# Kernel tuning notes

Measured on AMD Instinct MI355X. Metric: run time of the kernel, lower is better.

## Reference

```python
import jax, jax.numpy as jnp
import numpy as np

L, V, D, H, FF, MAXLEN = 6, 32000, 512, 8, 2048, 512
EPS = 1e-6


def _pos_encoding(max_len, d):
    pos = jnp.arange(max_len, dtype=jnp.float32)[:, None]            # [S,1]
    i = (jnp.floor(jnp.arange(d, dtype=jnp.float32) / 2) * 2) / d     # [D]
    inv = 1.0 / jnp.power(10000.0, i)
    em = pos * inv[None, :]                                           # [S,D]
    even = (jnp.arange(d) % 2) == 0
    return jnp.where(even[None, :], jnp.sin(em), jnp.cos(em))         # [S,D]


def _layernorm(x, g, b):
    mu = jnp.mean(x, axis=-1, keepdims=True)
    var = jnp.mean(jnp.square(x - mu), axis=-1, keepdims=True)
    return (x - mu) / jnp.sqrt(var + EPS) * g + b


def _mha(q_in, k_in, v_in, mask, w, b):
    # w: [4, D, D] torch-style [out,in] for q,k,v,o; b: [4, D]
    dh = D // H
    q = jnp.einsum('bsd,od->bso', q_in, w[0]) + b[0]
    k = jnp.einsum('bsd,od->bso', k_in, w[1]) + b[1]
    v = jnp.einsum('bsd,od->bso', v_in, w[2]) + b[2]
    split = lambda t: t.reshape(t.shape[0], t.shape[1], H, dh).transpose(0, 2, 1, 3)
    q, k, v = split(q), split(k), split(v)                            # [B,H,S,dh]
    s = jnp.einsum('bhqd,bhkd->bhqk', q, k) / jnp.sqrt(jnp.float32(dh))
    s = s - mask * 1e6
    a = jax.nn.softmax(s, axis=-1)
    o = jnp.einsum('bhqk,bhkd->bhqd', a, v)
    o = o.transpose(0, 2, 1, 3).reshape(o.shape[0], -1, D)
    return jnp.einsum('bsd,od->bso', o, w[3]) + b[3]


def setup_inputs() -> dict:
    key = jax.random.key(0)
    ks = jax.random.split(key, 20)
    B, S = 4, 512
    tokens = jax.random.randint(ks[0], (B, S), 0, V)
    en_out = jax.random.normal(ks[1], (B, S, D), dtype=jnp.float32)
    en_pad_mask = jnp.where(jax.random.uniform(ks[2], (B, 1, 1, S)) < 0.1, 1.0, 0.0).astype(jnp.float32)
    emb = jax.random.normal(ks[3], (V, D), dtype=jnp.float32) * 0.1
    emb = emb.at[0].set(0.0)  # padding_idx=0
    gain = 2.0 ** 0.5
    std_att = gain / np.sqrt(D)
    sa_w = jax.random.normal(ks[4], (L, 4, D, D), dtype=jnp.float32) * std_att
    sa_b = jnp.zeros((L, 4, D), dtype=jnp.float32)
    ca_w = jax.random.normal(ks[5], (L, 4, D, D), dtype=jnp.float32) * std_att
    ca_b = jnp.zeros((L, 4, D), dtype=jnp.float32)
    ff_w1 = jax.random.normal(ks[6], (L, FF, D), dtype=jnp.float32) * (gain / np.sqrt(D))
    ff_b1 = jnp.zeros((L, FF), dtype=jnp.float32)
    ff_w2 = jax.random.normal(ks[7], (L, D, FF), dtype=jnp.float32) * (gain / np.sqrt(FF))
    ff_b2 = jnp.zeros((L, D), dtype=jnp.float32)
    ln_g = jnp.ones((L, 3, D), dtype=jnp.float32)
    ln_b = jnp.zeros((L, 3, D), dtype=jnp.float32)
    out_w = jax.random.normal(ks[8], (V, D), dtype=jnp.float32) * np.sqrt(2.0 / (V + D))
    out_b = jnp.zeros((V,), dtype=jnp.float32)
    return dict(tokens=tokens, en_out=en_out, en_pad_mask=en_pad_mask, emb=emb,
                sa_w=sa_w, sa_b=sa_b, ca_w=ca_w, ca_b=ca_b,
                ff_w1=ff_w1, ff_b1=ff_b1, ff_w2=ff_w2, ff_b2=ff_b2,
                ln_g=ln_g, ln_b=ln_b, out_w=out_w, out_b=out_b)


def reference(tokens, en_out, en_pad_mask, emb, sa_w, sa_b, ca_w, ca_b,
              ff_w1, ff_b1, ff_w2, ff_b2, ln_g, ln_b, out_w, out_b):
    B, S = tokens.shape
    # decoder padding mask + lookahead mask
    de_pad = jnp.where(tokens == 0, 1.0, 0.0).reshape(B, 1, 1, S)
    tri = (1.0 - jnp.tril(jnp.ones((S, S), dtype=jnp.float32)))[None, None]  # [1,1,S,S]
    la_mask = jnp.maximum(de_pad, tri)                                        # [B,1,S,S]
    # embedding + positional encoding (dropout p given; inference -> identity)
    x = emb[tokens] * jnp.sqrt(jnp.float32(D)) + _pos_encoding(MAXLEN, D)[None, :S]
    for i in range(L):
        h = _layernorm(x + _mha(x, x, x, la_mask, sa_w[i], sa_b[i]), ln_g[i, 0], ln_b[i, 0])
        a = _layernorm(h + _mha(h, en_out, en_out, en_pad_mask, ca_w[i], ca_b[i]), ln_g[i, 1], ln_b[i, 1])
        ff = jnp.einsum('bsf,df->bsd', jax.nn.relu(jnp.einsum('bsd,fd->bsf', a, ff_w1[i]) + ff_b1[i]), ff_w2[i]) + ff_b2[i]
        x = _layernorm(a + ff, ln_g[i, 2], ln_b[i, 2])
    return jnp.einsum('bsd,vd->bsv', x, out_w) + out_b
```

## Files before the change

kernel.cpp:

```cpp
#include <hip/hip_runtime.h>
#include <math.h>

#define DMODEL 512
#define NHEAD  8
#define DHEAD  64
#define SEQ    512
#define BATCH  4
#define NLAYER 6
#define FFDIM  2048
#define VOCAB  32000

__global__ void embed_kernel(const int* __restrict__ tokens,
                             const float* __restrict__ emb,
                             float* __restrict__ x) {
    int idx = blockIdx.x;
    int s   = idx & (SEQ - 1);
    int tok = tokens[idx];
    const float scale = 22.627416997969522f;
    for (int d = threadIdx.x; d < DMODEL; d += blockDim.x) {
        float i2  = (float)((d >> 1) << 1) / (float)DMODEL;
        float inv = powf(10000.0f, -i2);
        float em  = (float)s * inv;
        float pe  = ((d & 1) == 0) ? sinf(em) : cosf(em);
        x[(size_t)idx * DMODEL + d] = emb[(size_t)tok * DMODEL + d] * scale + pe;
    }
}

__global__ __launch_bounds__(256) void gemm_bias_64(
        const float* __restrict__ A, const float* __restrict__ W,
        const float* __restrict__ bias, float* __restrict__ C,
        int M, int N, int K, int relu) {
    __shared__ float As[32][68];
    __shared__ float Bs[32][68];
    int bm  = blockIdx.x * 64;
    int bn  = blockIdx.y * 64;
    int tid = threadIdx.x;
    int tx  = tid & 15;
    int ty  = tid >> 4;
    int lrow = tid >> 2;
    int lq   = (tid & 3) << 2;

    const float* Ap = A + (size_t)(bm + lrow) * K + lq;
    const float* Wp = W + (size_t)(bn + lrow) * K + lq;

    float acc[4][4] = {};
    float4 av0 = *(const float4*)Ap;
    float4 av1 = *(const float4*)(Ap + 16);
    float4 wv0 = *(const float4*)Wp;
    float4 wv1 = *(const float4*)(Wp + 16);

    for (int k0 = 0; k0 < K; k0 += 32) {
        As[lq + 0][lrow]  = av0.x; As[lq + 1][lrow]  = av0.y;
        As[lq + 2][lrow]  = av0.z; As[lq + 3][lrow]  = av0.w;
        As[lq + 16][lrow] = av1.x; As[lq + 17][lrow] = av1.y;
        As[lq + 18][lrow] = av1.z; As[lq + 19][lrow] = av1.w;
        Bs[lq + 0][lrow]  = wv0.x; Bs[lq + 1][lrow]  = wv0.y;
        Bs[lq + 2][lrow]  = wv0.z; Bs[lq + 3][lrow]  = wv0.w;
        Bs[lq + 16][lrow] = wv1.x; Bs[lq + 17][lrow] = wv1.y;
        Bs[lq + 18][lrow] = wv1.z; Bs[lq + 19][lrow] = wv1.w;
        __syncthreads();
        int kn = (k0 + 32 < K) ? k0 + 32 : k0;
        av0 = *(const float4*)(Ap + kn);
        av1 = *(const float4*)(Ap + kn + 16);
        wv0 = *(const float4*)(Wp + kn);
        wv1 = *(const float4*)(Wp + kn + 16);
#pragma unroll
        for (int kk = 0; kk < 32; kk++) {
            float4 a = *(const float4*)&As[kk][ty * 4];
            float4 b = *(const float4*)&Bs[kk][tx * 4];
            float ar[4] = {a.x, a.y, a.z, a.w};
            float br[4] = {b.x, b.y, b.z, b.w};
#pragma unroll
            for (int i = 0; i < 4; i++)
#pragma unroll
                for (int j = 0; j < 4; j++) acc[i][j] += ar[i] * br[j];
        }
        __syncthreads();
    }

    float4 bv = *(const float4*)(bias + bn + tx * 4);
    float bb[4] = {bv.x, bv.y, bv.z, bv.w};
#pragma unroll
    for (int i = 0; i < 4; i++) {
        int row = bm + ty * 4 + i;
        float4 v;
        v.x = acc[i][0] + bb[0]; v.y = acc[i][1] + bb[1];
        v.z = acc[i][2] + bb[2]; v.w = acc[i][3] + bb[3];
        if (relu) {
            v.x = fmaxf(v.x, 0.f); v.y = fmaxf(v.y, 0.f);
            v.z = fmaxf(v.z, 0.f); v.w = fmaxf(v.w, 0.f);
        }
        *(float4*)(C + (size_t)row * N + bn + tx * 4) = v;
    }
}

__global__ __launch_bounds__(256) void gemm_bias_128(
        const float* __restrict__ A, const float* __restrict__ W,
        const float* __restrict__ bias, float* __restrict__ C,
        int M, int N, int K, int relu) {
    __shared__ float As[32][132];
    __shared__ float Bs[32][132];
    int bm  = blockIdx.x * 128;
    int bn  = blockIdx.y * 128;
    int tid = threadIdx.x;
    int tx  = tid & 15;
    int ty  = tid >> 4;
    int lrow = tid >> 2;
    int lq   = (tid & 3) << 2;

    const float* Ap  = A + (size_t)(bm + lrow) * K + lq;
    const float* Ap2 = Ap + (size_t)64 * K;
    const float* Wp  = W + (size_t)(bn + lrow) * K + lq;
    const float* Wp2 = Wp + (size_t)64 * K;

    float acc[8][8] = {};
    float4 a00 = *(const float4*)Ap;
    float4 a01 = *(const float4*)(Ap + 16);
    float4 a10 = *(const float4*)Ap2;
    float4 a11 = *(const float4*)(Ap2 + 16);
    float4 w00 = *(const float4*)Wp;
    float4 w01 = *(const float4*)(Wp + 16);
    float4 w10 = *(const float4*)Wp2;
    float4 w11 = *(const float4*)(Wp2 + 16);

    for (int k0 = 0; k0 < K; k0 += 32) {
        As[lq + 0][lrow]       = a00.x; As[lq + 1][lrow]       = a00.y;
        As[lq + 2][lrow]       = a00.z; As[lq + 3][lrow]       = a00.w;
        As[lq + 16][lrow]      = a01.x; As[lq + 17][lrow]      = a01.y;
        As[lq + 18][lrow]      = a01.z; As[lq + 19][lrow]      = a01.w;
        As[lq + 0][lrow + 64]  = a10.x; As[lq + 1][lrow + 64]  = a10.y;
        As[lq + 2][lrow + 64]  = a10.z; As[lq + 3][lrow + 64]  = a10.w;
        As[lq + 16][lrow + 64] = a11.x; As[lq + 17][lrow + 64] = a11.y;
        As[lq + 18][lrow + 64] = a11.z; As[lq + 19][lrow + 64] = a11.w;
        Bs[lq + 0][lrow]       = w00.x; Bs[lq + 1][lrow]       = w00.y;
        Bs[lq + 2][lrow]       = w00.z; Bs[lq + 3][lrow]       = w00.w;
        Bs[lq + 16][lrow]      = w01.x; Bs[lq + 17][lrow]      = w01.y;
        Bs[lq + 18][lrow]      = w01.z; Bs[lq + 19][lrow]      = w01.w;
        Bs[lq + 0][lrow + 64]  = w10.x; Bs[lq + 1][lrow + 64]  = w10.y;
        Bs[lq + 2][lrow + 64]  = w10.z; Bs[lq + 3][lrow + 64]  = w10.w;
        Bs[lq + 16][lrow + 64] = w11.x; Bs[lq + 17][lrow + 64] = w11.y;
        Bs[lq + 18][lrow + 64] = w11.z; Bs[lq + 19][lrow + 64] = w11.w;
        __syncthreads();
        int kn = (k0 + 32 < K) ? k0 + 32 : k0;
        a00 = *(const float4*)(Ap + kn);
        a01 = *(const float4*)(Ap + kn + 16);
        a10 = *(const float4*)(Ap2 + kn);
        a11 = *(const float4*)(Ap2 + kn + 16);
        w00 = *(const float4*)(Wp + kn);
        w01 = *(const float4*)(Wp + kn + 16);
        w10 = *(const float4*)(Wp2 + kn);
        w11 = *(const float4*)(Wp2 + kn + 16);
#pragma unroll
        for (int kk = 0; kk < 32; kk++) {
            float4 A0 = *(const float4*)&As[kk][ty * 4];
            float4 A1 = *(const float4*)&As[kk][ty * 4 + 64];
            float4 B0 = *(const float4*)&Bs[kk][tx * 4];
            float4 B1 = *(const float4*)&Bs[kk][tx * 4 + 64];
            float ar[8] = {A0.x, A0.y, A0.z, A0.w, A1.x, A1.y, A1.z, A1.w};
            float br[8] = {B0.x, B0.y, B0.z, B0.w, B1.x, B1.y, B1.z, B1.w};
#pragma unroll
            for (int i = 0; i < 8; i++)
#pragma unroll
                for (int j = 0; j < 8; j++) acc[i][j] += ar[i] * br[j];
        }
        __syncthreads();
    }

    float4 bv0 = *(const float4*)(bias + bn + tx * 4);
    float4 bv1 = *(const float4*)(bias + bn + tx * 4 + 64);
    float bb[8] = {bv0.x, bv0.y, bv0.z, bv0.w, bv1.x, bv1.y, bv1.z, bv1.w};
#pragma unroll
    for (int i = 0; i < 8; i++) {
        int row = bm + ty * 4 + (i & 3) + (i >> 2) * 64;
        float4 v0, v1;
        v0.x = acc[i][0] + bb[0]; v0.y = acc[i][1] + bb[1];
        v0.z = acc[i][2] + bb[2]; v0.w = acc[i][3] + bb[3];
        v1.x = acc[i][4] + bb[4]; v1.y = acc[i][5] + bb[5];
        v1.z = acc[i][6] + bb[6]; v1.w = acc[i][7] + bb[7];
        if (relu) {
            v0.x = fmaxf(v0.x, 0.f); v0.y = fmaxf(v0.y, 0.f);
            v0.z = fmaxf(v0.z, 0.f); v0.w = fmaxf(v0.w, 0.f);
            v1.x = fmaxf(v1.x, 0.f); v1.y = fmaxf(v1.y, 0.f);
            v1.z = fmaxf(v1.z, 0.f); v1.w = fmaxf(v1.w, 0.f);
        }
        float* crow = C + (size_t)row * N + bn + tx * 4;
        *(float4*)crow = v0;
        *(float4*)(crow + 64) = v1;
    }
}

__global__ __launch_bounds__(256) void attn_tile_kernel(
        const float* __restrict__ Q, const float* __restrict__ K,
        const float* __restrict__ Vv, const int* __restrict__ tokens,
        const float* __restrict__ en_pad, float* __restrict__ O,
        int ldq, int ldkv, int causal) {
    int qt  = blockIdx.x;
    int h   = blockIdx.y;
    int b   = blockIdx.z;
    int tid = threadIdx.x;
    int tx  = tid & 15;
    int ty  = tid >> 4;
    int lrow = tid >> 2;
    int lq4  = tid & 3;

    __shared__ float Qs[DHEAD][68];
    __shared__ float KP[64][68];
    __shared__ float Vs[64][72];

    {
        const float* qbase = Q + ((size_t)b * SEQ + qt * 64 + lrow) * ldq + h * DHEAD;
#pragma unroll
        for (int i = 0; i < 4; i++) {
            int dk = (lq4 + i * 4) * 4;
            float4 f = *(const float4*)(qbase + dk);
            Qs[dk + 0][lrow] = f.x; Qs[dk + 1][lrow] = f.y;
            Qs[dk + 2][lrow] = f.z; Qs[dk + 3][lrow] = f.w;
        }
    }

    float o[4][4] = {};
    float mrow[4] = {-INFINITY, -INFINITY, -INFINITY, -INFINITY};
    float lsum[4] = {0.f, 0.f, 0.f, 0.f};
    int nc = causal ? (qt + 1) : (SEQ / 64);

    for (int ct = 0; ct < nc; ct++) {
        __syncthreads();
        const float* kbase = K  + ((size_t)b * SEQ + ct * 64 + lrow) * ldkv + h * DHEAD;
        const float* vbase = Vv + ((size_t)b * SEQ + ct * 64 + lrow) * ldkv + h * DHEAD;
#pragma unroll
        for (int i = 0; i < 4; i++) {
            int dk = (lq4 + i * 4) * 4;
            float4 f = *(const float4*)(kbase + dk);
            KP[dk + 0][lrow] = f.x; KP[dk + 1][lrow] = f.y;
            KP[dk + 2][lrow] = f.z; KP[dk + 3][lrow] = f.w;
            float4 g = *(const float4*)(vbase + dk);
            *(float4*)&Vs[lrow][dk] = g;
        }
        __syncthreads();

        float s[4][4] = {};
#pragma unroll
        for (int d = 0; d < DHEAD; d++) {
            float4 a  = *(const float4*)&Qs[d][ty * 4];
            float4 bb = *(const float4*)&KP[d][tx * 4];
            float ar[4] = {a.x, a.y, a.z, a.w};
            float br[4] = {bb.x, bb.y, bb.z, bb.w};
#pragma unroll
            for (int i = 0; i < 4; i++)
#pragma unroll
                for (int j = 0; j < 4; j++) s[i][j] += ar[i] * br[j];
        }
        __syncthreads();

        float cmask[4];
#pragma unroll
        for (int j = 0; j < 4; j++) {
            int jg = ct * 64 + tx * 4 + j;
            cmask[j] = causal ? ((tokens[b * SEQ + jg] == 0) ? 1.0f : 0.0f)
                              : en_pad[b * SEQ + jg];
        }
#pragma unroll
        for (int i = 0; i < 4; i++) {
            int qg = qt * 64 + ty * 4 + i;
#pragma unroll
            for (int j = 0; j < 4; j++) {
                int jg = ct * 64 + tx * 4 + j;
                float mk = cmask[j];
                if (causal && jg > qg) mk = 1.0f;
                s[i][j] = s[i][j] * 0.125f - mk * 1.0e6f;
            }
        }

#pragma unroll
        for (int i = 0; i < 4; i++) {
            float rm = fmaxf(fmaxf(s[i][0], s[i][1]), fmaxf(s[i][2], s[i][3]));
#pragma unroll
            for (int msk = 1; msk < 16; msk <<= 1)
                rm = fmaxf(rm, __shfl_xor(rm, msk));
            float mn = fmaxf(mrow[i], rm);
            float sc = expf(mrow[i] - mn);
            mrow[i] = mn;
            float ps = 0.0f;
#pragma unroll
            for (int j = 0; j < 4; j++) {
                float p = expf(s[i][j] - mn);
                s[i][j] = p;
                ps += p;
            }
#pragma unroll
            for (int msk = 1; msk < 16; msk <<= 1)
                ps += __shfl_xor(ps, msk);
            lsum[i] = lsum[i] * sc + ps;
#pragma unroll
            for (int j = 0; j < 4; j++) o[i][j] *= sc;
        }

#pragma unroll
        for (int i = 0; i < 4; i++)
            *(float4*)&KP[ty * 4 + i][tx * 4] =
                make_float4(s[i][0], s[i][1], s[i][2], s[i][3]);
        __syncthreads();

#pragma unroll
        for (int k0 = 0; k0 < 64; k0 += 4) {
            float4 a0 = *(const float4*)&KP[ty * 4 + 0][k0];
            float4 a1 = *(const float4*)&KP[ty * 4 + 1][k0];
            float4 a2 = *(const float4*)&KP[ty * 4 + 2][k0];
            float4 a3 = *(const float4*)&KP[ty * 4 + 3][k0];
            float ar[4][4] = {{a0.x, a0.y, a0.z, a0.w},
                              {a1.x, a1.y, a1.z, a1.w},
                              {a2.x, a2.y, a2.z, a2.w},
                              {a3.x, a3.y, a3.z, a3.w}};
#pragma unroll
            for (int kk = 0; kk < 4; kk++) {
                float4 bv = *(const float4*)&Vs[k0 + kk][tx * 4];
                float br[4] = {bv.x, bv.y, bv.z, bv.w};
#pragma unroll
                for (int i = 0; i < 4; i++)
#pragma unroll
                    for (int j = 0; j < 4; j++) o[i][j] += ar[i][kk] * br[j];
            }
        }
    }

#pragma unroll
    for (int i = 0; i < 4; i++) {
        float inv = 1.0f / lsum[i];
        float4 v = make_float4(o[i][0] * inv, o[i][1] * inv,
                               o[i][2] * inv, o[i][3] * inv);
        *(float4*)(O + ((size_t)b * SEQ + qt * 64 + ty * 4 + i) * DMODEL
                   + h * DHEAD + tx * 4) = v;
    }
}

__global__ __launch_bounds__(64) void ln_res_kernel(
        const float* __restrict__ x, const float* __restrict__ y,
        const float* __restrict__ g, const float* __restrict__ b,
        float* __restrict__ out) {
    int row = blockIdx.x;
    int t   = threadIdx.x;
    size_t base = (size_t)row * DMODEL;
    const float4* x4 = (const float4*)(x + base);
    const float4* y4 = (const float4*)(y + base);
    float4 a0 = x4[t], a1 = x4[t + 64];
    float4 c0 = y4[t], c1 = y4[t + 64];
    float v0x = a0.x + c0.x, v0y = a0.y + c0.y, v0z = a0.z + c0.z, v0w = a0.w + c0.w;
    float v1x = a1.x + c1.x, v1y = a1.y + c1.y, v1z = a1.z + c1.z, v1w = a1.w + c1.w;

    float s = v0x + v0y + v0z + v0w + v1x + v1y + v1z + v1w;
#pragma unroll
    for (int m = 1; m < 64; m <<= 1) s += __shfl_xor(s, m);
    float mu = s * (1.0f / 512.0f);

    float d0x = v0x - mu, d0y = v0y - mu, d0z = v0z - mu, d0w = v0w - mu;
    float d1x = v1x - mu, d1y = v1y - mu, d1z = v1z - mu, d1w = v1w - mu;
    float q = d0x * d0x + d0y * d0y + d0z * d0z + d0w * d0w
            + d1x * d1x + d1y * d1y + d1z * d1z + d1w * d1w;
#pragma unroll
    for (int m = 1; m < 64; m <<= 1) q += __shfl_xor(q, m);
    float inv = rsqrtf(q * (1.0f / 512.0f) + 1e-6f);

    const float4* g4 = (const float4*)g;
    const float4* b4 = (const float4*)b;
    float4 gv0 = g4[t], gv1 = g4[t + 64];
    float4 bv0 = b4[t], bv1 = b4[t + 64];
    float4* o4 = (float4*)(out + base);
    o4[t]      = make_float4(d0x * inv * gv0.x + bv0.x, d0y * inv * gv0.y + bv0.y,
                             d0z * inv * gv0.z + bv0.z, d0w * inv * gv0.w + bv0.w);
    o4[t + 64] = make_float4(d1x * inv * gv1.x + bv1.x, d1y * inv * gv1.y + bv1.y,
                             d1z * inv * gv1.z + bv1.z, d1w * inv * gv1.w + bv1.w);
}

extern "C" void kernel_launch(void* const* d_in, const int* in_sizes, int n_in,
                              void* d_out, int out_size, void* d_ws, size_t ws_size,
                              hipStream_t stream) {
    const int*   tokens = (const int*)  d_in[0];
    const float* en_out = (const float*)d_in[1];
    const float* en_pad = (const float*)d_in[2];
    const float* emb    = (const float*)d_in[3];
    const float* sa_w   = (const float*)d_in[4];
    const float* sa_b   = (const float*)d_in[5];
    const float* ca_w   = (const float*)d_in[6];
    const float* ca_b   = (const float*)d_in[7];
    const float* ff_w1  = (const float*)d_in[8];
    const float* ff_b1  = (const float*)d_in[9];
    const float* ff_w2  = (const float*)d_in[10];
    const float* ff_b2  = (const float*)d_in[11];
    const float* ln_g   = (const float*)d_in[12];
    const float* ln_b   = (const float*)d_in[13];
    const float* out_w  = (const float*)d_in[14];
    const float* out_b  = (const float*)d_in[15];
    float* logits = (float*)d_out;

    const int BS = BATCH * SEQ;
    const size_t NTOK = (size_t)BS * DMODEL;

    float* ws   = (float*)d_ws;
    float* buf0 = ws;
    float* buf1 = ws + NTOK;
    float* qkv  = ws + 2 * NTOK;
    float* kv   = qkv + NTOK;
    float* att  = ws + 5 * NTOK;
    float* proj = ws + 6 * NTOK;
    float* ffb  = ws + 7 * NTOK;

    dim3 g_qkv(BS / 64, 3 * DMODEL / 64);
    dim3 g_dd(BS / 64, DMODEL / 64);
    dim3 g_kv(BS / 64, 2 * DMODEL / 64);
    dim3 g_ff1(BS / 128, FFDIM / 128);
    dim3 g_vocab(BS / 128, VOCAB / 128);
    dim3 attn_grid(SEQ / 64, NHEAD, BATCH);

    embed_kernel<<<BS, 256, 0, stream>>>(tokens, emb, buf0);

    float* cur = buf0;
    float* oth = buf1;
    for (int l = 0; l < NLAYER; l++) {
        const float* sw = sa_w + (size_t)l * 4 * DMODEL * DMODEL;
        const float* sb = sa_b + (size_t)l * 4 * DMODEL;
        const float* cw = ca_w + (size_t)l * 4 * DMODEL * DMODEL;
        const float* cb = ca_b + (size_t)l * 4 * DMODEL;
        const float* lg = ln_g + (size_t)l * 3 * DMODEL;
        const float* lb = ln_b + (size_t)l * 3 * DMODEL;

        gemm_bias_64<<<g_qkv, 256, 0, stream>>>(cur, sw, sb, qkv, BS, 3 * DMODEL, DMODEL, 0);
        attn_tile_kernel<<<attn_grid, 256, 0, stream>>>(qkv, qkv + DMODEL, qkv + 2 * DMODEL,
                                                        tokens, nullptr, att,
                                                        3 * DMODEL, 3 * DMODEL, 1);
        gemm_bias_64<<<g_dd, 256, 0, stream>>>(att, sw + 3 * DMODEL * DMODEL, sb + 3 * DMODEL,
                                               proj, BS, DMODEL, DMODEL, 0);
        ln_res_kernel<<<BS, 64, 0, stream>>>(cur, proj, lg, lb, oth);

        gemm_bias_64<<<g_dd, 256, 0, stream>>>(oth, cw, cb, qkv, BS, DMODEL, DMODEL, 0);
        gemm_bias_64<<<g_kv, 256, 0, stream>>>(en_out, cw + DMODEL * DMODEL, cb + DMODEL,
                                               kv, BS, 2 * DMODEL, DMODEL, 0);
        attn_tile_kernel<<<attn_grid, 256, 0, stream>>>(qkv, kv, kv + DMODEL,
                                                        tokens, en_pad, att,
                                                        DMODEL, 2 * DMODEL, 0);
        gemm_bias_64<<<g_dd, 256, 0, stream>>>(att, cw + 3 * DMODEL * DMODEL, cb + 3 * DMODEL,
                                               proj, BS, DMODEL, DMODEL, 0);
        ln_res_kernel<<<BS, 64, 0, stream>>>(oth, proj, lg + DMODEL, lb + DMODEL, cur);

        gemm_bias_128<<<g_ff1, 256, 0, stream>>>(cur, ff_w1 + (size_t)l * FFDIM * DMODEL,
                                                 ff_b1 + (size_t)l * FFDIM, ffb,
                                                 BS, FFDIM, DMODEL, 1);
        gemm_bias_64<<<g_dd, 256, 0, stream>>>(ffb, ff_w2 + (size_t)l * DMODEL * FFDIM,
                                               ff_b2 + (size_t)l * DMODEL, proj,
                                               BS, DMODEL, FFDIM, 0);
        ln_res_kernel<<<BS, 64, 0, stream>>>(cur, proj, lg + 2 * DMODEL, lb + 2 * DMODEL, oth);

        float* t2 = cur; cur = oth; oth = t2;
    }

    gemm_bias_128<<<g_vocab, 256, 0, stream>>>(cur, out_w, out_b, logits, BS, VOCAB, DMODEL, 0);
}
```

Measured before the change: 4.029 ms.

## Use split-bf16 MFMA GEMM for wide projections, FFN1 and vocab

Adds a GEMM kernel that splits each fp32 operand into three bf16 parts and accumulates six cross-product MFMA 16x16x32 bf16 instructions, emulating near-fp32 precision on matrix cores. It replaces the scalar FMA GEMMs for the QKV, cross-attention KV, FFN first layer and vocabulary projections, where most of the FLOPs are. The aim is to move the dominant matrix work onto MFMA units. The cost is the extra splitting ALU work, a larger LDS footprint and a store epilogue that writes scalars with strided access instead of float4.

```diff
diff --git a/kernel.cpp b/kernel.cpp
--- a/kernel.cpp
+++ b/kernel.cpp
@@ -9,6 +9,11 @@
 #define NLAYER 6
 #define FFDIM  2048
 #define VOCAB  32000
+
+using bf16x8 = __attribute__((ext_vector_type(8))) __bf16;
+using f32x4  = __attribute__((ext_vector_type(4))) float;
+typedef unsigned int uint32;
+typedef unsigned short ushort16;
 
 __global__ void embed_kernel(const int* __restrict__ tokens,
                              const float* __restrict__ emb,
@@ -26,6 +31,139 @@
     }
 }
 
+__device__ __forceinline__ void split3(float x, ushort16& s0, ushort16& s1, ushort16& s2) {
+    uint32 u0 = __builtin_bit_cast(uint32, x);
+    s0 = (ushort16)(u0 >> 16);
+    float r1 = x - __builtin_bit_cast(float, u0 & 0xffff0000u);
+    uint32 u1 = __builtin_bit_cast(uint32, r1);
+    s1 = (ushort16)(u1 >> 16);
+    float r2 = r1 - __builtin_bit_cast(float, u1 & 0xffff0000u);
+    s2 = (ushort16)(__builtin_bit_cast(uint32, r2) >> 16);
+}
+
+#define LDSP 40
+__global__ __launch_bounds__(256, 2) void gemm_mfma3(
+        const float* __restrict__ A, const float* __restrict__ W,
+        const float* __restrict__ bias, float* __restrict__ C,
+        int M, int N, int K, int relu) {
+    __shared__ ushort16 As[3][128][LDSP];
+    __shared__ ushort16 Bs[3][128][LDSP];
+    int bm  = blockIdx.x * 128;
+    int bn  = blockIdx.y * 128;
+    int tid = threadIdx.x;
+    int w   = tid >> 6;
+    int l   = tid & 63;
+    int wrow = (w >> 1) * 64;
+    int wcol = (w & 1) * 64;
+    int r2  = tid >> 2;
+    int qq  = tid & 3;
+
+    const float* Abase = A + (size_t)(bm + r2) * K + qq * 4;
+    const float* Wbase = W + (size_t)(bn + r2) * K + qq * 4;
+    const size_t rowK64 = (size_t)64 * K;
+
+    f32x4 acc[4][4];
+#pragma unroll
+    for (int i = 0; i < 4; i++)
+#pragma unroll
+        for (int j = 0; j < 4; j++) acc[i][j] = (f32x4){0.f, 0.f, 0.f, 0.f};
+
+    float4 va[4], vw[4];
+#pragma unroll
+    for (int c = 0; c < 4; c++) {
+        size_t off = (size_t)(c >> 1) * rowK64 + (c & 1) * 16;
+        va[c] = *(const float4*)(Abase + off);
+        vw[c] = *(const float4*)(Wbase + off);
+    }
+
+    for (int k0 = 0; k0 < K; k0 += 32) {
+#pragma unroll
+        for (int c = 0; c < 4; c++) {
+            int row = r2 + ((c >> 1) << 6);
+            int kb  = (qq << 2) + ((c & 1) << 4);
+            float xa[4] = {va[c].x, va[c].y, va[c].z, va[c].w};
+            float xw[4] = {vw[c].x, vw[c].y, vw[c].z, vw[c].w};
+            ushort16 a0[4], a1[4], a2[4], w0[4], w1[4], w2[4];
+#pragma unroll
+            for (int e = 0; e < 4; e++) {
+                split3(xa[e], a0[e], a1[e], a2[e]);
+                split3(xw[e], w0[e], w1[e], w2[e]);
+            }
+            *(uint32*)&As[0][row][kb]     = (uint32)a0[0] | ((uint32)a0[1] << 16);
+            *(uint32*)&As[0][row][kb + 2] = (uint32)a0[2] | ((uint32)a0[3] << 16);
+            *(uint32*)&As[1][row][kb]     = (uint32)a1[0] | ((uint32)a1[1] << 16);
+            *(uint32*)&As[1][row][kb + 2] = (uint32)a1[2] | ((uint32)a1[3] << 16);
+            *(uint32*)&As[2][row][kb]     = (uint32)a2[0] | ((uint32)a2[1] << 16);
+            *(uint32*)&As[2][row][kb + 2] = (uint32)a2[2] | ((uint32)a2[3] << 16);
+            *(uint32*)&Bs[0][row][kb]     = (uint32)w0[0] | ((uint32)w0[1] << 16);
+            *(uint32*)&Bs[0][row][kb + 2] = (uint32)w0[2] | ((uint32)w0[3] << 16);
+            *(uint32*)&Bs[1][row][kb]     = (uint32)w1[0] | ((uint32)w1[1] << 16);
+            *(uint32*)&Bs[1][row][kb + 2] = (uint32)w1[2] | ((uint32)w1[3] << 16);
+            *(uint32*)&Bs[2][row][kb]     = (uint32)w2[0] | ((uint32)w2[1] << 16);
+            *(uint32*)&Bs[2][row][kb + 2] = (uint32)w2[2] | ((uint32)w2[3] << 16);
+        }
+        __syncthreads();
+
+        if (k0 + 32 < K) {
+#pragma unroll
+            for (int c = 0; c < 4; c++) {
+                size_t off = (size_t)(c >> 1) * rowK64 + (c & 1) * 16 + k0 + 32;
+                va[c] = *(const float4*)(Abase + off);
+                vw[c] = *(const float4*)(Wbase + off);
+            }
+        }
+
+        int fr = l & 15;
+        int kg = (l >> 4) * 8;
+        bf16x8 bf[3][4];
+#pragma unroll
+        for (int nj = 0; nj < 4; nj++) {
+            int rowb = wcol + nj * 16 + fr;
+            bf[0][nj] = *(const bf16x8*)&Bs[0][rowb][kg];
+            bf[1][nj] = *(const bf16x8*)&Bs[1][rowb][kg];
+            bf[2][nj] = *(const bf16x8*)&Bs[2][rowb][kg];
+        }
+#pragma unroll
+        for (int mi = 0; mi < 4; mi++) {
+            int rowa = wrow + mi * 16 + fr;
+            bf16x8 af0 = *(const bf16x8*)&As[0][rowa][kg];
+            bf16x8 af1 = *(const bf16x8*)&As[1][rowa][kg];
+            bf16x8 af2 = *(const bf16x8*)&As[2][rowa][kg];
+#pragma unroll
+            for (int nj = 0; nj < 4; nj++) {
+                f32x4 a = acc[mi][nj];
+                a = __builtin_amdgcn_mfma_f32_16x16x32_bf16(af2, bf[0][nj], a, 0, 0, 0);
+                a = __builtin_amdgcn_mfma_f32_16x16x32_bf16(af1, bf[1][nj], a, 0, 0, 0);
+                a = __builtin_amdgcn_mfma_f32_16x16x32_bf16(af0, bf[2][nj], a, 0, 0, 0);
+                a = __builtin_amdgcn_mfma_f32_16x16x32_bf16(af1, bf[0][nj], a, 0, 0, 0);
+                a = __builtin_amdgcn_mfma_f32_16x16x32_bf16(af0, bf[1][nj], a, 0, 0, 0);
+                a = __builtin_amdgcn_mfma_f32_16x16x32_bf16(af0, bf[0][nj], a, 0, 0, 0);
+                acc[mi][nj] = a;
+            }
+        }
+        __syncthreads();
+    }
+
+    int cl = l & 15;
+    int rh = (l >> 4) * 4;
+#pragma unroll
+    for (int nj = 0; nj < 4; nj++) {
+        int col = bn + wcol + nj * 16 + cl;
+        float bv = bias[col];
+#pragma unroll
+        for (int mi = 0; mi < 4; mi++) {
+            f32x4 a = acc[mi][nj];
+            int rbase = bm + wrow + mi * 16 + rh;
+#pragma unroll
+            for (int r = 0; r < 4; r++) {
+                float v = a[r] + bv;
+                if (relu) v = fmaxf(v, 0.0f);
+                C[(size_t)(rbase + r) * N + col] = v;
+            }
+        }
+    }
+}
+
 __global__ __launch_bounds__(256) void gemm_bias_64(
         const float* __restrict__ A, const float* __restrict__ W,
         const float* __restrict__ bias, float* __restrict__ C,
@@ -91,101 +229,6 @@
             v.z = fmaxf(v.z, 0.f); v.w = fmaxf(v.w, 0.f);
         }
         *(float4*)(C + (size_t)row * N + bn + tx * 4) = v;
-    }
-}
-
-__global__ __launch_bounds__(256) void gemm_bias_128(
-        const float* __restrict__ A, const float* __restrict__ W,
-        const float* __restrict__ bias, float* __restrict__ C,
-        int M, int N, int K, int relu) {
-    __shared__ float As[32][132];
-    __shared__ float Bs[32][132];
-    int bm  = blockIdx.x * 128;
-    int bn  = blockIdx.y * 128;
-    int tid = threadIdx.x;
-    int tx  = tid & 15;
-    int ty  = tid >> 4;
-    int lrow = tid >> 2;
-    int lq   = (tid & 3) << 2;
-
-    const float* Ap  = A + (size_t)(bm + lrow) * K + lq;
-    const float* Ap2 = Ap + (size_t)64 * K;
-    const float* Wp  = W + (size_t)(bn + lrow) * K + lq;
-    const float* Wp2 = Wp + (size_t)64 * K;
-
-    float acc[8][8] = {};
-    float4 a00 = *(const float4*)Ap;
-    float4 a01 = *(const float4*)(Ap + 16);
-    float4 a10 = *(const float4*)Ap2;
-    float4 a11 = *(const float4*)(Ap2 + 16);
-    float4 w00 = *(const float4*)Wp;
-    float4 w01 = *(const float4*)(Wp + 16);
-    float4 w10 = *(const float4*)Wp2;
-    float4 w11 = *(const float4*)(Wp2 + 16);
-
-    for (int k0 = 0; k0 < K; k0 += 32) {
-        As[lq + 0][lrow]       = a00.x; As[lq + 1][lrow]       = a00.y;
-        As[lq + 2][lrow]       = a00.z; As[lq + 3][lrow]       = a00.w;
-        As[lq + 16][lrow]      = a01.x; As[lq + 17][lrow]      = a01.y;
-        As[lq + 18][lrow]      = a01.z; As[lq + 19][lrow]      = a01.w;
-        As[lq + 0][lrow + 64]  = a10.x; As[lq + 1][lrow + 64]  = a10.y;
-        As[lq + 2][lrow + 64]  = a10.z; As[lq + 3][lrow + 64]  = a10.w;
-        As[lq + 16][lrow + 64] = a11.x; As[lq + 17][lrow + 64] = a11.y;
-        As[lq + 18][lrow + 64] = a11.z; As[lq + 19][lrow + 64] = a11.w;
-        Bs[lq + 0][lrow]       = w00.x; Bs[lq + 1][lrow]       = w00.y;
-        Bs[lq + 2][lrow]       = w00.z; Bs[lq + 3][lrow]       = w00.w;
-        Bs[lq + 16][lrow]      = w01.x; Bs[lq + 17][lrow]      = w01.y;
-        Bs[lq + 18][lrow]      = w01.z; Bs[lq + 19][lrow]      = w01.w;
-        Bs[lq + 0][lrow + 64]  = w10.x; Bs[lq + 1][lrow + 64]  = w10.y;
-        Bs[lq + 2][lrow + 64]  = w10.z; Bs[lq + 3][lrow + 64]  = w10.w;
-        Bs[lq + 16][lrow + 64] = w11.x; Bs[lq + 17][lrow + 64] = w11.y;
-        Bs[lq + 18][lrow + 64] = w11.z; Bs[lq + 19][lrow + 64] = w11.w;
-        __syncthreads();
-        int kn = (k0 + 32 < K) ? k0 + 32 : k0;
-        a00 = *(const float4*)(Ap + kn);
-        a01 = *(const float4*)(Ap + kn + 16);
-        a10 = *(const float4*)(Ap2 + kn);
-        a11 = *(const float4*)(Ap2 + kn + 16);
-        w00 = *(const float4*)(Wp + kn);
-        w01 = *(const float4*)(Wp + kn + 16);
-        w10 = *(const float4*)(Wp2 + kn);
-        w11 = *(const float4*)(Wp2 + kn + 16);
-#pragma unroll
-        for (int kk = 0; kk < 32; kk++) {
-            float4 A0 = *(const float4*)&As[kk][ty * 4];
-            float4 A1 = *(const float4*)&As[kk][ty * 4 + 64];
-            float4 B0 = *(const float4*)&Bs[kk][tx * 4];
-            float4 B1 = *(const float4*)&Bs[kk][tx * 4 + 64];
-            float ar[8] = {A0.x, A0.y, A0.z, A0.w, A1.x, A1.y, A1.z, A1.w};
-            float br[8] = {B0.x, B0.y, B0.z, B0.w, B1.x, B1.y, B1.z, B1.w};
-#pragma unroll
-            for (int i = 0; i < 8; i++)
-#pragma unroll
-                for (int j = 0; j < 8; j++) acc[i][j] += ar[i] * br[j];
-        }
-        __syncthreads();
-    }
-
-    float4 bv0 = *(const float4*)(bias + bn + tx * 4);
-    float4 bv1 = *(const float4*)(bias + bn + tx * 4 + 64);
-    float bb[8] = {bv0.x, bv0.y, bv0.z, bv0.w, bv1.x, bv1.y, bv1.z, bv1.w};
-#pragma unroll
-    for (int i = 0; i < 8; i++) {
-        int row = bm + ty * 4 + (i & 3) + (i >> 2) * 64;
-        float4 v0, v1;
-        v0.x = acc[i][0] + bb[0]; v0.y = acc[i][1] + bb[1];
-        v0.z = acc[i][2] + bb[2]; v0.w = acc[i][3] + bb[3];
-        v1.x = acc[i][4] + bb[4]; v1.y = acc[i][5] + bb[5];
-        v1.z = acc[i][6] + bb[6]; v1.w = acc[i][7] + bb[7];
-        if (relu) {
-            v0.x = fmaxf(v0.x, 0.f); v0.y = fmaxf(v0.y, 0.f);
-            v0.z = fmaxf(v0.z, 0.f); v0.w = fmaxf(v0.w, 0.f);
-            v1.x = fmaxf(v1.x, 0.f); v1.y = fmaxf(v1.y, 0.f);
-            v1.z = fmaxf(v1.z, 0.f); v1.w = fmaxf(v1.w, 0.f);
-        }
-        float* crow = C + (size_t)row * N + bn + tx * 4;
-        *(float4*)crow = v0;
-        *(float4*)(crow + 64) = v1;
     }
 }
 
@@ -404,11 +447,11 @@
     float* proj = ws + 6 * NTOK;
     float* ffb  = ws + 7 * NTOK;
 
-    dim3 g_qkv(BS / 64, 3 * DMODEL / 64);
+    dim3 gm_qkv(BS / 128, 3 * DMODEL / 128);
+    dim3 gm_kv(BS / 128, 2 * DMODEL / 128);
+    dim3 gm_ff1(BS / 128, FFDIM / 128);
+    dim3 gm_vocab(BS / 128, VOCAB / 128);
     dim3 g_dd(BS / 64, DMODEL / 64);
-    dim3 g_kv(BS / 64, 2 * DMODEL / 64);
-    dim3 g_ff1(BS / 128, FFDIM / 128);
-    dim3 g_vocab(BS / 128, VOCAB / 128);
     dim3 attn_grid(SEQ / 64, NHEAD, BATCH);
 
     embed_kernel<<<BS, 256, 0, stream>>>(tokens, emb, buf0);
@@ -423,7 +466,7 @@
         const float* lg = ln_g + (size_t)l * 3 * DMODEL;
         const float* lb = ln_b + (size_t)l * 3 * DMODEL;
 
-        gemm_bias_64<<<g_qkv, 256, 0, stream>>>(cur, sw, sb, qkv, BS, 3 * DMODEL, DMODEL, 0);
+        gemm_mfma3<<<gm_qkv, 256, 0, stream>>>(cur, sw, sb, qkv, BS, 3 * DMODEL, DMODEL, 0);
         attn_tile_kernel<<<attn_grid, 256, 0, stream>>>(qkv, qkv + DMODEL, qkv + 2 * DMODEL,
                                                         tokens, nullptr, att,
                                                         3 * DMODEL, 3 * DMODEL, 1);
@@ -432,8 +475,8 @@
         ln_res_kernel<<<BS, 64, 0, stream>>>(cur, proj, lg, lb, oth);
 
         gemm_bias_64<<<g_dd, 256, 0, stream>>>(oth, cw, cb, qkv, BS, DMODEL, DMODEL, 0);
-        gemm_bias_64<<<g_kv, 256, 0, stream>>>(en_out, cw + DMODEL * DMODEL, cb + DMODEL,
-                                               kv, BS, 2 * DMODEL, DMODEL, 0);
+        gemm_mfma3<<<gm_kv, 256, 0, stream>>>(en_out, cw + DMODEL * DMODEL, cb + DMODEL,
+                                              kv, BS, 2 * DMODEL, DMODEL, 0);
         attn_tile_kernel<<<attn_grid, 256, 0, stream>>>(qkv, kv, kv + DMODEL,
                                                         tokens, en_pad, att,
                                                         DMODEL, 2 * DMODEL, 0);
@@ -441,9 +484,9 @@
                                                proj, BS, DMODEL, DMODEL, 0);
         ln_res_kernel<<<BS, 64, 0, stream>>>(oth, proj, lg + DMODEL, lb + DMODEL, cur);
 
-        gemm_bias_128<<<g_ff1, 256, 0, stream>>>(cur, ff_w1 + (size_t)l * FFDIM * DMODEL,
-                                                 ff_b1 + (size_t)l * FFDIM, ffb,
-                                                 BS, FFDIM, DMODEL, 1);
+        gemm_mfma3<<<gm_ff1, 256, 0, stream>>>(cur, ff_w1 + (size_t)l * FFDIM * DMODEL,
+                                               ff_b1 + (size_t)l * FFDIM, ffb,
+                                               BS, FFDIM, DMODEL, 1);
         gemm_bias_64<<<g_dd, 256, 0, stream>>>(ffb, ff_w2 + (size_t)l * DMODEL * FFDIM,
                                                ff_b2 + (size_t)l * DMODEL, proj,
                                                BS, DMODEL, FFDIM, 0);
@@ -452,5 +495,5 @@
         float* t2 = cur; cur = oth; oth = t2;
     }
 
-    gemm_bias_128<<<g_vocab, 256, 0, stream>>>(cur, out_w, out_b, logits, BS, VOCAB, DMODEL, 0);
-}
+    gemm_mfma3<<<gm_vocab, 256, 0, stream>>>(cur, out_w, out_b, logits, BS, VOCAB, DMODEL, 0);
+}
```

Result: faster. 3.471 ms (-13.8%).
